# Kernel tuning notes

Measured on AMD Instinct MI355X. Metric: run time of the kernel, lower is better.

The kernel has to match this reference:

```python
import math
import jax, jax.numpy as jnp
import numpy as np

HEADS = 16
DIM_HEAD = 64
BSZ = 16        # block_size
EPS = 1e-8


def _flip_every_two(t):
    # t: (B, nblk, z, d) -> flip adjacent pairs along nblk
    B, nblk = t.shape[0], t.shape[1]
    t = t.reshape(B, nblk // 2, 2, *t.shape[2:])
    t = jnp.flip(t, axis=2)
    return t.reshape(B, nblk, *t.shape[3:])


def setup_inputs() -> dict:
    key = jax.random.key(0)
    k1, k2, k3 = jax.random.split(key, 3)
    b, n, dim = 4, 8192, 1024
    inner = HEADS * DIM_HEAD
    x = jax.random.normal(k1, (b, n, dim), dtype=jnp.float32)
    w_qkv = jax.random.normal(k2, (dim, inner * 3), dtype=jnp.float32) * 0.02
    w_out = jax.random.normal(k3, (inner, dim), dtype=jnp.float32) * 0.02
    b_out = jnp.zeros((dim,), dtype=jnp.float32)
    return {"x": x, "w_qkv": w_qkv, "w_out": w_out, "b_out": b_out}


def _hattention(x, w_qkv, w_out, b_out):
    b, n, dim = x.shape  # n assumed power of 2 -> no padding needed
    scale = DIM_HEAD ** -0.5

    qkv = x @ w_qkv                                   # (b, n, 3*inner)
    q, k, v = jnp.split(qkv, 3, axis=-1)

    def to_heads(t):
        return t.reshape(b, n, HEADS, DIM_HEAD).transpose(0, 2, 1, 3).reshape(b * HEADS, n, DIM_HEAD)

    q, k, v = map(to_heads, (q, k, v))
    q = q * scale

    num_levels = int(math.log2(n // BSZ)) - 1

    # build coarsened pyramid: q,k averaged over pairs, v summed
    qkvs = [(q, k, v)]
    for _ in range(num_levels):
        B, m, d = q.shape
        q = q.reshape(B, m // 2, 2, d).mean(axis=2)
        k = k.reshape(B, m // 2, 2, d).mean(axis=2)
        v = v.reshape(B, m // 2, 2, d).sum(axis=2)
        qkvs.append((q, k, v))

    def to_blocks(t):
        return t.reshape(t.shape[0], -1, BSZ, DIM_HEAD)

    Ys = []
    L = len(qkvs)
    for ind, (ql, kl, vl) in enumerate(reversed(qkvs)):
        is_last = ind == L - 1
        qb, kb, vb = map(to_blocks, (ql, kl, vl))
        if not is_last:
            kb = _flip_every_two(kb)
            vb = _flip_every_two(vb)
        # block-local unnormalized softmax attention
        S = jnp.einsum('bnid,bnjd->bnij', qb, kb)
        S = S - jnp.max(S, axis=-1, keepdims=True)
        A = jnp.exp(S)
        y = jnp.einsum('bnij,bnjd->bnid', A, vb)
        Asum = A.sum(axis=-1)
        Ys.append((y.reshape(y.shape[0], -1, DIM_HEAD),
                   Asum.reshape(Asum.shape[0], -1)))

    # combine coarse-to-fine by upsampling (repeat by 2) and summing
    Y, A = Ys[0]
    for Yl, Al in Ys[1:]:
        Y = jnp.repeat(Y, 2, axis=1) + Yl
        A = jnp.repeat(A, 2, axis=1) + Al

    out = Y / (A + EPS)[..., None]                    # (b*h, n, d)
    out = out.reshape(b, HEADS, n, DIM_HEAD).transpose(0, 2, 1, 3).reshape(b, n, HEADS * DIM_HEAD)
    return out @ w_out + b_out


def reference(x, w_qkv, w_out, b_out):
    return _hattention(x, w_qkv, w_out, b_out)
```

## Files before the change

### kernel.cpp

```cpp
#include <hip/hip_runtime.h>
#include <hip/hip_bf16.h>

typedef __bf16 bf16_t;
typedef bf16_t bf16x8 __attribute__((ext_vector_type(8)));
typedef float f32x4 __attribute__((ext_vector_type(4)));

#define PROWS 16352

__device__ __forceinline__ void gl_lds16(const bf16_t* g, bf16_t* l) {
  __builtin_amdgcn_global_load_lds(
      (const __attribute__((address_space(1))) void*)g,
      (__attribute__((address_space(3))) void*)l,
      16, 0, 0);
}

__device__ __forceinline__ void load8f(const bf16_t* p, float* f) {
  bf16x8 v = *(const bf16x8*)p;
#pragma unroll
  for (int e = 0; e < 8; ++e) f[e] = (float)v[e];
}
__device__ __forceinline__ void store8f(bf16_t* p, const float* f) {
  bf16x8 v;
#pragma unroll
  for (int e = 0; e < 8; ++e) v[e] = (bf16_t)f[e];
  *(bf16x8*)p = v;
}

__global__ __launch_bounds__(256) void cvt_f32_to_bf16(const float* __restrict__ in,
                                                       bf16_t* __restrict__ o) {
  size_t gid = (size_t)blockIdx.x * 256 + threadIdx.x;
  const float4* p = (const float4*)in + gid * 2;
  float4 a = p[0], b = p[1];
  bf16x8 v;
  v[0] = (bf16_t)a.x; v[1] = (bf16_t)a.y; v[2] = (bf16_t)a.z; v[3] = (bf16_t)a.w;
  v[4] = (bf16_t)b.x; v[5] = (bf16_t)b.y; v[6] = (bf16_t)b.z; v[7] = (bf16_t)b.w;
  *(bf16x8*)(o + gid * 8) = v;
}

__global__ __launch_bounds__(256) void transpose_to_bf16(const float* __restrict__ w,
                                                         bf16_t* __restrict__ wT,
                                                         int K, int N) {
  __shared__ float t[32][33];
  int bx = blockIdx.x, by = blockIdx.y;
  int tx = threadIdx.x & 31, ty = threadIdx.x >> 5;
#pragma unroll
  for (int r = ty; r < 32; r += 8)
    t[r][tx] = w[(size_t)(by * 32 + r) * N + bx * 32 + tx];
  __syncthreads();
#pragma unroll
  for (int r = ty; r < 32; r += 8)
    wT[(size_t)(bx * 32 + r) * K + by * 32 + tx] = (bf16_t)t[tx][r];
}

template <int EPI>
__global__ __launch_bounds__(512, 2) void gemm256p(const bf16_t* __restrict__ A,
                                                   const bf16_t* __restrict__ Bt,
                                                   float* __restrict__ Cp,
                                                   const float* __restrict__ bias,
                                                   bf16_t* __restrict__ Pq,
                                                   bf16_t* __restrict__ Pk,
                                                   bf16_t* __restrict__ Pv,
                                                   int ldc, int nTilesN, int tilesPerBlock) {
  __shared__ __align__(16) bf16_t As[2 * 256 * 64];
  __shared__ __align__(16) bf16_t Bs[2 * 256 * 64];
  const int LD = 1024;
  const int tid = threadIdx.x;
  const int w = tid >> 6, lane = tid & 63;

  const int chunk = (blockIdx.x & 7) * 32 + (blockIdx.x >> 3);
  const int tile0 = chunk * tilesPerBlock;
  const int nSteps = tilesPerBlock * 16;

  const int wr = w >> 2, wc = w & 3;
  const int lr = lane & 15, lg = lane >> 4;
  const int sw = lr & 7;
  f32x4 acc[8][4] = {};

  auto stageHalf = [&](const bf16_t* __restrict__ G, int rbase, int kt,
                       bf16_t* lbuf, int h) {
#pragma unroll
    for (int j = 0; j < 2; ++j) {
      int b = j * 8 + w;
      int r3 = lane >> 3;
      int k8 = (lane & 7) ^ r3;
      gl_lds16(G + (size_t)(rbase + h * 128 + b * 8 + r3) * LD + kt + k8 * 8,
               lbuf + h * 8192 + b * 512);
    }
  };

  {
    int mt = tile0 / nTilesN, nt0 = tile0 % nTilesN;
    int bm = mt * 256, bn = nt0 * 256;
    stageHalf(Bt, bn, 0, Bs, 0); stageHalf(Bt, bn, 0, Bs, 1);
    stageHalf(A, bm, 0, As, 0);  stageHalf(A, bm, 0, As, 1);
    stageHalf(Bt, bn, 64, Bs + 16384, 0); stageHalf(Bt, bn, 64, Bs + 16384, 1);
    stageHalf(A, bm, 64, As + 16384, 0);  stageHalf(A, bm, 64, As + 16384, 1);
    asm volatile("s_waitcnt vmcnt(8)" ::: "memory");
  }
  __syncthreads();

  for (int g = 0; g < nSteps; ++g) {
    const int tile = tile0 + (g >> 4);
    const int ktl = g & 15;
    const int c = g & 1;
    bf16_t* Abuf = As + c * 16384;
    bf16_t* Bbuf = Bs + c * 16384;
    const int g2 = g + 2;
    const bool pf = g2 < nSteps;
    const int t2 = tile0 + (g2 >> 4);
    const int mt2 = t2 / nTilesN, nt2v = t2 % nTilesN;
    const int bm2 = mt2 * 256, bn2 = nt2v * 256;
    const int kt2 = (g2 & 15) << 6;
    bf16x8 bfrag[4][2];

#pragma unroll
    for (int p = 0; p < 4; ++p) {
      bf16x8 afrag[2][2];
#pragma unroll
      for (int fi = 0; fi < 2; ++fi)
#pragma unroll
        for (int kk = 0; kk < 2; ++kk)
          afrag[fi][kk] = *(const bf16x8*)&Abuf[(wr * 128 + p * 32 + fi * 16 + lr) * 64 +
                                                (((kk * 4 + lg) ^ sw) * 8)];
      if (p == 0) {
#pragma unroll
        for (int fj = 0; fj < 4; ++fj)
#pragma unroll
          for (int kk = 0; kk < 2; ++kk)
            bfrag[fj][kk] = *(const bf16x8*)&Bbuf[(wc * 64 + fj * 16 + lr) * 64 +
                                                  (((kk * 4 + lg) ^ sw) * 8)];
      }
      if (pf) {
        if (p == 1) stageHalf(Bt, bn2, kt2, Bbuf, 0);
        if (p == 2) stageHalf(Bt, bn2, kt2, Bbuf, 1);
        if (p == 3) { stageHalf(A, bm2, kt2, Abuf, 0); stageHalf(A, bm2, kt2, Abuf, 1); }
      }
      __builtin_amdgcn_s_barrier();
      asm volatile("s_waitcnt lgkmcnt(0)" ::: "memory");
      __builtin_amdgcn_sched_barrier(0);
      __builtin_amdgcn_s_setprio(1);
#pragma unroll
      for (int kk = 0; kk < 2; ++kk)
#pragma unroll
        for (int fi = 0; fi < 2; ++fi)
#pragma unroll
          for (int fj = 0; fj < 4; ++fj)
            acc[p * 2 + fi][fj] = __builtin_amdgcn_mfma_f32_16x16x32_bf16(
                afrag[fi][kk], bfrag[fj][kk], acc[p * 2 + fi][fj], 0, 0, 0);
      __builtin_amdgcn_s_setprio(0);
      if (p == 3) {
        if (pf) asm volatile("s_waitcnt vmcnt(8)" ::: "memory");
        else    asm volatile("s_waitcnt vmcnt(0)" ::: "memory");
      }
      __builtin_amdgcn_s_barrier();
    }

    if (ktl == 15) {
      const int mt = tile / nTilesN, ntv = tile % nTilesN;
      const int bm = mt * 256, bn = ntv * 256;
      if (EPI == 1) {
        float bv[4];
#pragma unroll
        for (int fj = 0; fj < 4; ++fj) bv[fj] = bias[bn + wc * 64 + fj * 16 + lr];
#pragma unroll
        for (int fi = 0; fi < 8; ++fi)
#pragma unroll
          for (int fj = 0; fj < 4; ++fj)
#pragma unroll
            for (int r = 0; r < 4; ++r) {
              int row = bm + wr * 128 + fi * 16 + lg * 4 + r;
              int col = bn + wc * 64 + fj * 16 + lr;
              Cp[(size_t)row * ldc + col] = acc[fi][fj][r] + bv[fj];
            }
      } else {
#pragma unroll
        for (int fi = 0; fi < 8; ++fi)
#pragma unroll
          for (int fj = 0; fj < 4; ++fj)
#pragma unroll
            for (int r = 0; r < 4; ++r) {
              int row = bm + wr * 128 + fi * 16 + lg * 4 + r;
              int col = bn + wc * 64 + fj * 16 + lr;
              float v = acc[fi][fj][r];
              int tns = col >> 10, col10 = col & 1023;
              int h = col10 >> 6, d = col10 & 63;
              int hg = (row >> 13) * 16 + h;
              int trow = row & 8191;
              if (tns == 0) v *= 0.125f;
              bf16_t* Pt = (tns == 0) ? Pq : (tns == 1 ? Pk : Pv);
              Pt[((size_t)hg * PROWS + trow) * 64 + d] = (bf16_t)v;
            }
      }
#pragma unroll
      for (int fi = 0; fi < 8; ++fi)
#pragma unroll
        for (int fj = 0; fj < 4; ++fj) acc[fi][fj] = (f32x4){};
    }
  }
}

__global__ __launch_bounds__(512) void coarsen_tree(bf16_t* __restrict__ Pq,
                                                    bf16_t* __restrict__ Pk,
                                                    bf16_t* __restrict__ Pv) {
  __shared__ float l6s[8][64];
  const int poffA[9] = {0, 8192, 12288, 14336, 15360, 15872, 16128, 16256, 16320};
  const int hg = blockIdx.x >> 4, win = blockIdx.x & 15;
  const int tid = threadIdx.x;
  const int d8 = tid & 7;
  const int tb = tid >> 3;
  const int wv = tid >> 6;
  const size_t base = (size_t)hg * PROWS;
  const int r0 = win * 512 + tb * 8;

#pragma unroll 1
  for (int tensor = 0; tensor < 3; ++tensor) {
    bf16_t* P = (tensor == 0) ? Pq : (tensor == 1 ? Pk : Pv);
    const float sc = (tensor == 2) ? 1.f : 0.5f;
    float v[8][8];
#pragma unroll
    for (int i = 0; i < 8; ++i) load8f(P + (base + r0 + i) * 64 + d8 * 8, v[i]);
    float a1[4][8];
#pragma unroll
    for (int i = 0; i < 4; ++i) {
#pragma unroll
      for (int e = 0; e < 8; ++e) a1[i][e] = sc * (v[2 * i][e] + v[2 * i + 1][e]);
      store8f(P + (base + poffA[1] + win * 256 + tb * 4 + i) * 64 + d8 * 8, a1[i]);
    }
    float a2[2][8];
#pragma unroll
    for (int i = 0; i < 2; ++i) {
#pragma unroll
      for (int e = 0; e < 8; ++e) a2[i][e] = sc * (a1[2 * i][e] + a1[2 * i + 1][e]);
      store8f(P + (base + poffA[2] + win * 128 + tb * 2 + i) * 64 + d8 * 8, a2[i]);
    }
    float a3[8];
#pragma unroll
    for (int e = 0; e < 8; ++e) a3[e] = sc * (a2[0][e] + a2[1][e]);
    store8f(P + (base + poffA[3] + win * 64 + tb) * 64 + d8 * 8, a3);
    float a4[8];
#pragma unroll
    for (int e = 0; e < 8; ++e) a4[e] = sc * (a3[e] + __shfl_xor(a3[e], 8, 64));
    if ((tb & 1) == 0) store8f(P + (base + poffA[4] + win * 32 + (tb >> 1)) * 64 + d8 * 8, a4);
    float a5[8];
#pragma unroll
    for (int e = 0; e < 8; ++e) a5[e] = sc * (a4[e] + __shfl_xor(a4[e], 16, 64));
    if ((tb & 3) == 0) store8f(P + (base + poffA[5] + win * 16 + (tb >> 2)) * 64 + d8 * 8, a5);
    float a6[8];
#pragma unroll
    for (int e = 0; e < 8; ++e) a6[e] = sc * (a5[e] + __shfl_xor(a5[e], 32, 64));
    if ((tb & 7) == 0) {
      bf16x8 o;
#pragma unroll
      for (int e = 0; e < 8; ++e) { l6s[wv][d8 * 8 + e] = a6[e]; o[e] = (bf16_t)a6[e]; }
      *(bf16x8*)(P + (base + poffA[6] + win * 8 + wv) * 64 + d8 * 8) = o;
    }
    __syncthreads();
    if (tid < 32) {
      int pr = tid >> 3;
      float a7[8];
#pragma unroll
      for (int e = 0; e < 8; ++e)
        a7[e] = sc * (l6s[2 * pr][d8 * 8 + e] + l6s[2 * pr + 1][d8 * 8 + e]);
      store8f(P + (base + poffA[7] + win * 4 + pr) * 64 + d8 * 8, a7);
      if (pr < 2) {
        float a8[8];
#pragma unroll
        for (int e = 0; e < 8; ++e)
          a8[e] = sc * (sc * (l6s[4 * pr][d8 * 8 + e] + l6s[4 * pr + 1][d8 * 8 + e]) +
                        sc * (l6s[4 * pr + 2][d8 * 8 + e] + l6s[4 * pr + 3][d8 * 8 + e]));
        store8f(P + (base + poffA[8] + win * 2 + pr) * 64 + d8 * 8, a8);
      }
    }
    __syncthreads();
  }
}

__global__ __launch_bounds__(256) void attn_all(bf16_t* __restrict__ Pq,
                                                const bf16_t* __restrict__ Pk,
                                                const bf16_t* __restrict__ Pv,
                                                float* __restrict__ Asum) {
  const int poffA[9] = {0, 8192, 12288, 14336, 15360, 15872, 16128, 16256, 16320};
  const int tid = threadIdx.x;
  const int wv = tid >> 6, lane = tid & 63;
  const int lr = lane & 15, lg = lane >> 4;

  int bid = blockIdx.x * 4 + wv;
  int l = 0, cnt = 32768;
  while (bid >= cnt) { bid -= cnt; cnt >>= 1; ++l; }
  const int lg2nblk = 9 - l;
  const int blk = bid & ((1 << lg2nblk) - 1);
  const int hg = bid >> lg2nblk;
  const int kvblk = l ? (blk ^ 1) : blk;
  const size_t qbase = (size_t)hg * PROWS + poffA[l] + blk * 16;
  const size_t kvbase = (size_t)hg * PROWS + poffA[l] + kvblk * 16;

  f32x4 s = {};
#pragma unroll
  for (int c = 0; c < 2; ++c) {
    bf16x8 ak = *(const bf16x8*)(Pk + (kvbase + lr) * 64 + c * 32 + lg * 8);
    bf16x8 bq = *(const bf16x8*)(Pq + (qbase + lr) * 64 + c * 32 + lg * 8);
    s = __builtin_amdgcn_mfma_f32_16x16x32_bf16(ak, bq, s, 0, 0, 0);
  }

  float mx = fmaxf(fmaxf(s[0], s[1]), fmaxf(s[2], s[3]));
  mx = fmaxf(mx, __shfl_xor(mx, 16, 64));
  mx = fmaxf(mx, __shfl_xor(mx, 32, 64));
  float a[4];
  float asum = 0.f;
#pragma unroll
  for (int r = 0; r < 4; ++r) {
    a[r] = (float)(bf16_t)__expf(s[r] - mx);
    asum += a[r];
  }
  asum += __shfl_xor(asum, 16, 64);
  asum += __shfl_xor(asum, 32, 64);
  if (lg == 0) Asum[qbase + lr] = asum;

  const int src0 = (2 * lg) * 16 + lr;
  const int src1 = (2 * lg + 1) * 16 + lr;
  bf16x8 pa;
#pragma unroll
  for (int r = 0; r < 4; ++r) {
    float c0 = __shfl(a[r], src0, 64);
    float c1 = __shfl(a[r], src1, 64);
    pa[r]     = (lg < 2) ? (bf16_t)c0 : (bf16_t)0.f;
    pa[r + 4] = (lg < 2) ? (bf16_t)c1 : (bf16_t)0.f;
  }

#pragma unroll
  for (int dt = 0; dt < 4; ++dt) {
    bf16x8 vf;
    if (lg < 2) {
#pragma unroll
      for (int e = 0; e < 8; ++e)
        vf[e] = Pv[(kvbase + lg * 8 + e) * 64 + dt * 16 + lr];
    } else {
#pragma unroll
      for (int e = 0; e < 8; ++e) vf[e] = (bf16_t)0.f;
    }
    f32x4 y = __builtin_amdgcn_mfma_f32_16x16x32_bf16(pa, vf, (f32x4){}, 0, 0, 0);
#pragma unroll
    for (int r = 0; r < 4; ++r)
      Pq[(qbase + 4 * lg + r) * 64 + dt * 16 + lr] = (bf16_t)y[r];
  }
}

__global__ __launch_bounds__(256) void combine_kernel(const bf16_t* __restrict__ Py,
                                                      const float* __restrict__ As,
                                                      bf16_t* __restrict__ attnb) {
  int gid = blockIdx.x * 256 + threadIdx.x;
  int d8 = gid & 7;
  int t = (gid >> 3) & 8191;
  int hg = gid >> 16;
  const int poffA[9] = {0, 8192, 12288, 14336, 15360, 15872, 16128, 16256, 16320};
  float acc[8] = {};
  float asum = 0.f;
#pragma unroll
  for (int l = 0; l < 9; ++l) {
    int rc = t >> l;
    size_t row = (size_t)hg * PROWS + poffA[l] + rc;
    asum += As[row];
    bf16x8 v = *(const bf16x8*)(Py + row * 64 + d8 * 8);
#pragma unroll
    for (int e = 0; e < 8; ++e) acc[e] += (float)v[e];
  }
  float inv = 1.f / (asum + 1e-8f);
  bf16x8 v;
#pragma unroll
  for (int e = 0; e < 8; ++e) v[e] = (bf16_t)(acc[e] * inv);
  *(bf16x8*)(attnb + ((size_t)(hg >> 4) * 8192 + t) * 1024 + (hg & 15) * 64 + d8 * 8) = v;
}

extern "C" void kernel_launch(void* const* d_in, const int* in_sizes, int n_in,
                              void* d_out, int out_size, void* d_ws, size_t ws_size,
                              hipStream_t stream) {
  const float* x = (const float*)d_in[0];
  const float* wqkv = (const float*)d_in[1];
  const float* wout = (const float*)d_in[2];
  const float* bout = (const float*)d_in[3];
  float* out = (float*)d_out;
  (void)in_sizes; (void)n_in; (void)out_size; (void)ws_size;

  char* base = (char*)d_ws;
  bf16_t* Pq    = (bf16_t*)(base + 0);
  bf16_t* Pk    = (bf16_t*)(base + 133955584);
  bf16_t* Pv    = (bf16_t*)(base + 267911168);
  float*  Ab    = (float*)(base + 401866752);
  bf16_t* woutT = (bf16_t*)(base + 406052864);
  bf16_t* x_bf  = (bf16_t*)(base + 408150016);
  bf16_t* wqkvT = (bf16_t*)(base + 475258880);
  bf16_t* attnb = (bf16_t*)(base + 133955584);

  cvt_f32_to_bf16<<<16384, 256, 0, stream>>>(x, x_bf);
  transpose_to_bf16<<<dim3(96, 32), 256, 0, stream>>>(wqkv, wqkvT, 1024, 3072);
  transpose_to_bf16<<<dim3(32, 32), 256, 0, stream>>>(wout, woutT, 1024, 1024);

  gemm256p<0><<<256, 512, 0, stream>>>(x_bf, wqkvT, nullptr, nullptr, Pq, Pk, Pv,
                                       3072, 12, 6);

  coarsen_tree<<<1024, 512, 0, stream>>>(Pq, Pk, Pv);

  attn_all<<<16352, 256, 0, stream>>>(Pq, Pk, Pv, Ab);
  combine_kernel<<<16384, 256, 0, stream>>>(Pq, Ab, attnb);

  gemm256p<1><<<256, 512, 0, stream>>>(attnb, woutT, out, bout, nullptr, nullptr, nullptr,
                                       1024, 4, 2);
}
```

Measured before the change: 585.6 us.

## Fuse fine-level attention with combine via LDS and simplify GEMM index math

Attention for the four finest pyramid levels now runs in the same kernel as the combine step. Per-block outputs and row sums stay in shared memory instead of being written to and reread from global memory. Only the coarse levels 4-8 keep a separate small attention kernel. The QKV GEMM also replaces per-step div/mod tile indexing with incremental counters and hoists the scatter-epilogue address math out of the inner loops. attnb moves to the x_bf region because Pk is now still read when combine writes its output.

```diff
diff --git a/kernel.cpp b/kernel.cpp
--- a/kernel.cpp
+++ b/kernel.cpp
@@ -88,29 +88,22 @@
     }
   };
 
-  {
-    int mt = tile0 / nTilesN, nt0 = tile0 % nTilesN;
-    int bm = mt * 256, bn = nt0 * 256;
-    stageHalf(Bt, bn, 0, Bs, 0); stageHalf(Bt, bn, 0, Bs, 1);
-    stageHalf(A, bm, 0, As, 0);  stageHalf(A, bm, 0, As, 1);
-    stageHalf(Bt, bn, 64, Bs + 16384, 0); stageHalf(Bt, bn, 64, Bs + 16384, 1);
-    stageHalf(A, bm, 64, As + 16384, 0);  stageHalf(A, bm, 64, As + 16384, 1);
-    asm volatile("s_waitcnt vmcnt(8)" ::: "memory");
-  }
+  int ntEc = tile0 % nTilesN;
+  int bmE = (tile0 / nTilesN) * 256, bnE = ntEc * 256;
+  int nt2c = ntEc, bm2 = bmE, bn2 = bnE, kt2 = 128;
+
+  stageHalf(Bt, bnE, 0, Bs, 0); stageHalf(Bt, bnE, 0, Bs, 1);
+  stageHalf(A, bmE, 0, As, 0);  stageHalf(A, bmE, 0, As, 1);
+  stageHalf(Bt, bnE, 64, Bs + 16384, 0); stageHalf(Bt, bnE, 64, Bs + 16384, 1);
+  stageHalf(A, bmE, 64, As + 16384, 0);  stageHalf(A, bmE, 64, As + 16384, 1);
+  asm volatile("s_waitcnt vmcnt(8)" ::: "memory");
   __syncthreads();
 
   for (int g = 0; g < nSteps; ++g) {
-    const int tile = tile0 + (g >> 4);
-    const int ktl = g & 15;
     const int c = g & 1;
     bf16_t* Abuf = As + c * 16384;
     bf16_t* Bbuf = Bs + c * 16384;
-    const int g2 = g + 2;
-    const bool pf = g2 < nSteps;
-    const int t2 = tile0 + (g2 >> 4);
-    const int mt2 = t2 / nTilesN, nt2v = t2 % nTilesN;
-    const int bm2 = mt2 * 256, bn2 = nt2v * 256;
-    const int kt2 = (g2 & 15) << 6;
+    const bool pf = (g + 2) < nSteps;
     bf16x8 bfrag[4][2];
 
 #pragma unroll
@@ -155,46 +148,51 @@
       __builtin_amdgcn_s_barrier();
     }
 
-    if (ktl == 15) {
-      const int mt = tile / nTilesN, ntv = tile % nTilesN;
-      const int bm = mt * 256, bn = ntv * 256;
+    kt2 += 64;
+    if (kt2 == 1024) {
+      kt2 = 0; ++nt2c; bn2 += 256;
+      if (nt2c == nTilesN) { nt2c = 0; bn2 = 0; bm2 += 256; }
+    }
+
+    if ((g & 15) == 15) {
       if (EPI == 1) {
         float bv[4];
 #pragma unroll
-        for (int fj = 0; fj < 4; ++fj) bv[fj] = bias[bn + wc * 64 + fj * 16 + lr];
+        for (int fj = 0; fj < 4; ++fj) bv[fj] = bias[bnE + wc * 64 + fj * 16 + lr];
 #pragma unroll
         for (int fi = 0; fi < 8; ++fi)
 #pragma unroll
           for (int fj = 0; fj < 4; ++fj)
 #pragma unroll
             for (int r = 0; r < 4; ++r) {
-              int row = bm + wr * 128 + fi * 16 + lg * 4 + r;
-              int col = bn + wc * 64 + fj * 16 + lr;
+              int row = bmE + wr * 128 + fi * 16 + lg * 4 + r;
+              int col = bnE + wc * 64 + fj * 16 + lr;
               Cp[(size_t)row * ldc + col] = acc[fi][fj][r] + bv[fj];
             }
       } else {
-#pragma unroll
-        for (int fi = 0; fi < 8; ++fi)
-#pragma unroll
-          for (int fj = 0; fj < 4; ++fj)
-#pragma unroll
-            for (int r = 0; r < 4; ++r) {
-              int row = bm + wr * 128 + fi * 16 + lg * 4 + r;
-              int col = bn + wc * 64 + fj * 16 + lr;
-              float v = acc[fi][fj][r];
-              int tns = col >> 10, col10 = col & 1023;
-              int h = col10 >> 6, d = col10 & 63;
-              int hg = (row >> 13) * 16 + h;
-              int trow = row & 8191;
-              if (tns == 0) v *= 0.125f;
-              bf16_t* Pt = (tns == 0) ? Pq : (tns == 1 ? Pk : Pv);
-              Pt[((size_t)hg * PROWS + trow) * 64 + d] = (bf16_t)v;
-            }
+        const int trow0 = (bmE & 8191) + wr * 128 + lg * 4;
+        const int hgRow = (bmE >> 13) << 4;
+#pragma unroll
+        for (int fj = 0; fj < 4; ++fj) {
+          int col = bnE + wc * 64 + fj * 16 + lr;
+          int tns = col >> 10, col10 = col & 1023;
+          int h = col10 >> 6, d = col10 & 63;
+          bf16_t* Pt = (tns == 0) ? Pq : (tns == 1 ? Pk : Pv);
+          bf16_t* bp = Pt + ((size_t)(hgRow + h) * PROWS + trow0) * 64 + d;
+          float scl = (tns == 0) ? 0.125f : 1.f;
+#pragma unroll
+          for (int fi = 0; fi < 8; ++fi)
+#pragma unroll
+            for (int r = 0; r < 4; ++r)
+              bp[(fi * 16 + r) * 64] = (bf16_t)(acc[fi][fj][r] * scl);
+        }
       }
 #pragma unroll
       for (int fi = 0; fi < 8; ++fi)
 #pragma unroll
         for (int fj = 0; fj < 4; ++fj) acc[fi][fj] = (f32x4){};
+      ++ntEc; bnE += 256;
+      if (ntEc == nTilesN) { ntEc = 0; bnE = 0; bmE += 256; }
     }
   }
 }
@@ -275,22 +273,23 @@
   }
 }
 
-__global__ __launch_bounds__(256) void attn_all(bf16_t* __restrict__ Pq,
-                                                const bf16_t* __restrict__ Pk,
-                                                const bf16_t* __restrict__ Pv,
-                                                float* __restrict__ Asum) {
+
+__global__ __launch_bounds__(256) void attn_hi(bf16_t* __restrict__ Pq,
+                                               const bf16_t* __restrict__ Pk,
+                                               const bf16_t* __restrict__ Pv,
+                                               float* __restrict__ Asum) {
   const int poffA[9] = {0, 8192, 12288, 14336, 15360, 15872, 16128, 16256, 16320};
   const int tid = threadIdx.x;
   const int wv = tid >> 6, lane = tid & 63;
   const int lr = lane & 15, lg = lane >> 4;
 
   int bid = blockIdx.x * 4 + wv;
-  int l = 0, cnt = 32768;
+  int l = 4, cnt = 2048;
   while (bid >= cnt) { bid -= cnt; cnt >>= 1; ++l; }
   const int lg2nblk = 9 - l;
   const int blk = bid & ((1 << lg2nblk) - 1);
   const int hg = bid >> lg2nblk;
-  const int kvblk = l ? (blk ^ 1) : blk;
+  const int kvblk = blk ^ 1;
   const size_t qbase = (size_t)hg * PROWS + poffA[l] + blk * 16;
   const size_t kvbase = (size_t)hg * PROWS + poffA[l] + kvblk * 16;
 
@@ -301,17 +300,12 @@
     bf16x8 bq = *(const bf16x8*)(Pq + (qbase + lr) * 64 + c * 32 + lg * 8);
     s = __builtin_amdgcn_mfma_f32_16x16x32_bf16(ak, bq, s, 0, 0, 0);
   }
-
   float mx = fmaxf(fmaxf(s[0], s[1]), fmaxf(s[2], s[3]));
   mx = fmaxf(mx, __shfl_xor(mx, 16, 64));
   mx = fmaxf(mx, __shfl_xor(mx, 32, 64));
-  float a[4];
-  float asum = 0.f;
-#pragma unroll
-  for (int r = 0; r < 4; ++r) {
-    a[r] = (float)(bf16_t)__expf(s[r] - mx);
-    asum += a[r];
-  }
+  float a[4]; float asum = 0.f;
+#pragma unroll
+  for (int r = 0; r < 4; ++r) { a[r] = (float)(bf16_t)__expf(s[r] - mx); asum += a[r]; }
   asum += __shfl_xor(asum, 16, 64);
   asum += __shfl_xor(asum, 32, 64);
   if (lg == 0) Asum[qbase + lr] = asum;
@@ -326,14 +320,12 @@
     pa[r]     = (lg < 2) ? (bf16_t)c0 : (bf16_t)0.f;
     pa[r + 4] = (lg < 2) ? (bf16_t)c1 : (bf16_t)0.f;
   }
-
 #pragma unroll
   for (int dt = 0; dt < 4; ++dt) {
     bf16x8 vf;
     if (lg < 2) {
 #pragma unroll
-      for (int e = 0; e < 8; ++e)
-        vf[e] = Pv[(kvbase + lg * 8 + e) * 64 + dt * 16 + lr];
+      for (int e = 0; e < 8; ++e) vf[e] = Pv[(kvbase + lg * 8 + e) * 64 + dt * 16 + lr];
     } else {
 #pragma unroll
       for (int e = 0; e < 8; ++e) vf[e] = (bf16_t)0.f;
@@ -345,30 +337,108 @@
   }
 }
 
-__global__ __launch_bounds__(256) void combine_kernel(const bf16_t* __restrict__ Py,
-                                                      const float* __restrict__ As,
-                                                      bf16_t* __restrict__ attnb) {
-  int gid = blockIdx.x * 256 + threadIdx.x;
-  int d8 = gid & 7;
-  int t = (gid >> 3) & 8191;
-  int hg = gid >> 16;
+__global__ __launch_bounds__(256) void attn_comb(const bf16_t* __restrict__ Pq,
+                                                 const bf16_t* __restrict__ Pk,
+                                                 const bf16_t* __restrict__ Pv,
+                                                 const float* __restrict__ Ab,
+                                                 bf16_t* __restrict__ attnb) {
+  __shared__ __align__(16) bf16_t yl[480 * 72];
+  __shared__ float asl[480];
   const int poffA[9] = {0, 8192, 12288, 14336, 15360, 15872, 16128, 16256, 16320};
-  float acc[8] = {};
-  float asum = 0.f;
-#pragma unroll
-  for (int l = 0; l < 9; ++l) {
-    int rc = t >> l;
-    size_t row = (size_t)hg * PROWS + poffA[l] + rc;
-    asum += As[row];
-    bf16x8 v = *(const bf16x8*)(Py + row * 64 + d8 * 8);
-#pragma unroll
-    for (int e = 0; e < 8; ++e) acc[e] += (float)v[e];
-  }
-  float inv = 1.f / (asum + 1e-8f);
-  bf16x8 v;
-#pragma unroll
-  for (int e = 0; e < 8; ++e) v[e] = (bf16_t)(acc[e] * inv);
-  *(bf16x8*)(attnb + ((size_t)(hg >> 4) * 8192 + t) * 1024 + (hg & 15) * 64 + d8 * 8) = v;
+  const int loffA[4] = {0, 256, 384, 448};
+  const int hg = blockIdx.x >> 5, win = blockIdx.x & 31;
+  const int tid = threadIdx.x;
+  const int wv = tid >> 6, lane = tid & 63;
+  const int lr = lane & 15, lg = lane >> 4;
+
+  auto do_attn = [&](int l, int blkL) {
+    const int nb = 16 >> l;
+    const int blk = win * nb + blkL;
+    const int kvblk = l ? (blk ^ 1) : blk;
+    const size_t qbase = (size_t)hg * PROWS + poffA[l] + (size_t)blk * 16;
+    const size_t kvbase = (size_t)hg * PROWS + poffA[l] + (size_t)kvblk * 16;
+    const int lrow = loffA[l] + blkL * 16;
+
+    f32x4 s = {};
+#pragma unroll
+    for (int c = 0; c < 2; ++c) {
+      bf16x8 ak = *(const bf16x8*)(Pk + (kvbase + lr) * 64 + c * 32 + lg * 8);
+      bf16x8 bq = *(const bf16x8*)(Pq + (qbase + lr) * 64 + c * 32 + lg * 8);
+      s = __builtin_amdgcn_mfma_f32_16x16x32_bf16(ak, bq, s, 0, 0, 0);
+    }
+    float mx = fmaxf(fmaxf(s[0], s[1]), fmaxf(s[2], s[3]));
+    mx = fmaxf(mx, __shfl_xor(mx, 16, 64));
+    mx = fmaxf(mx, __shfl_xor(mx, 32, 64));
+    float a[4]; float asum = 0.f;
+#pragma unroll
+    for (int r = 0; r < 4; ++r) { a[r] = (float)(bf16_t)__expf(s[r] - mx); asum += a[r]; }
+    asum += __shfl_xor(asum, 16, 64);
+    asum += __shfl_xor(asum, 32, 64);
+    if (lg == 0) asl[lrow + lr] = asum;
+
+    const int src0 = (2 * lg) * 16 + lr;
+    const int src1 = (2 * lg + 1) * 16 + lr;
+    bf16x8 pa;
+#pragma unroll
+    for (int r = 0; r < 4; ++r) {
+      float c0 = __shfl(a[r], src0, 64);
+      float c1 = __shfl(a[r], src1, 64);
+      pa[r]     = (lg < 2) ? (bf16_t)c0 : (bf16_t)0.f;
+      pa[r + 4] = (lg < 2) ? (bf16_t)c1 : (bf16_t)0.f;
+    }
+#pragma unroll
+    for (int dt = 0; dt < 4; ++dt) {
+      bf16x8 vf;
+      if (lg < 2) {
+#pragma unroll
+        for (int e = 0; e < 8; ++e) vf[e] = Pv[(kvbase + lg * 8 + e) * 64 + dt * 16 + lr];
+      } else {
+#pragma unroll
+        for (int e = 0; e < 8; ++e) vf[e] = (bf16_t)0.f;
+      }
+      f32x4 y = __builtin_amdgcn_mfma_f32_16x16x32_bf16(pa, vf, (f32x4){}, 0, 0, 0);
+#pragma unroll
+      for (int r = 0; r < 4; ++r)
+        yl[(lrow + 4 * lg + r) * 72 + dt * 16 + lr] = (bf16_t)y[r];
+    }
+  };
+
+  do_attn(0, wv * 4 + 0); do_attn(0, wv * 4 + 1);
+  do_attn(0, wv * 4 + 2); do_attn(0, wv * 4 + 3);
+  do_attn(1, wv * 2 + 0); do_attn(1, wv * 2 + 1);
+  do_attn(2, wv);
+  if (wv < 2) do_attn(3, wv);
+  __syncthreads();
+
+  const int d8 = tid & 7, rg = tid >> 3;
+#pragma unroll
+  for (int i = 0; i < 8; ++i) {
+    const int r = rg * 8 + i;
+    const int t = win * 256 + r;
+    float acc[8] = {};
+    float asum = 0.f;
+#pragma unroll
+    for (int l = 0; l < 4; ++l) {
+      const int row = loffA[l] + (r >> l);
+      asum += asl[row];
+      bf16x8 v = *(const bf16x8*)&yl[row * 72 + d8 * 8];
+#pragma unroll
+      for (int e = 0; e < 8; ++e) acc[e] += (float)v[e];
+    }
+#pragma unroll
+    for (int l = 4; l < 9; ++l) {
+      const size_t grow = (size_t)hg * PROWS + poffA[l] + (t >> l);
+      asum += Ab[grow];
+      bf16x8 v = *(const bf16x8*)(Pq + grow * 64 + d8 * 8);
+#pragma unroll
+      for (int e = 0; e < 8; ++e) acc[e] += (float)v[e];
+    }
+    const float inv = 1.f / (asum + 1e-8f);
+    bf16x8 o;
+#pragma unroll
+    for (int e = 0; e < 8; ++e) o[e] = (bf16_t)(acc[e] * inv);
+    *(bf16x8*)(attnb + ((size_t)(hg >> 4) * 8192 + t) * 1024 + (hg & 15) * 64 + d8 * 8) = o;
+  }
 }
 
 extern "C" void kernel_launch(void* const* d_in, const int* in_sizes, int n_in,
@@ -389,7 +459,7 @@
   bf16_t* woutT = (bf16_t*)(base + 406052864);
   bf16_t* x_bf  = (bf16_t*)(base + 408150016);
   bf16_t* wqkvT = (bf16_t*)(base + 475258880);
-  bf16_t* attnb = (bf16_t*)(base + 133955584);
+  bf16_t* attnb = (bf16_t*)(base + 408150016);
 
   cvt_f32_to_bf16<<<16384, 256, 0, stream>>>(x, x_bf);
   transpose_to_bf16<<<dim3(96, 32), 256, 0, stream>>>(wqkv, wqkvT, 1024, 3072);
@@ -400,8 +470,8 @@
 
   coarsen_tree<<<1024, 512, 0, stream>>>(Pq, Pk, Pv);
 
-  attn_all<<<16352, 256, 0, stream>>>(Pq, Pk, Pv, Ab);
-  combine_kernel<<<16384, 256, 0, stream>>>(Pq, Ab, attnb);
+  attn_hi<<<992, 256, 0, stream>>>(Pq, Pk, Pv, Ab);
+  attn_comb<<<2048, 256, 0, stream>>>(Pq, Pk, Pv, Ab, attnb);
 
   gemm256p<1><<<256, 512, 0, stream>>>(attnb, woutT, out, bout, nullptr, nullptr, nullptr,
                                        1024, 4, 2);
```

Result: no change. 592.7 us (+1.2%).
